# Kernel tuning notes

Hardware: AMD Instinct MI355X
Metric: run time of the kernel (lower is better)

Reference implementation:

```python
import jax, jax.numpy as jnp
import numpy as np
from jax import lax

B, C_IN, T_IN = 1024, 22, 2047
C_TEMP, KT, PAD = 20, 12, 6
N_PATCH = 8
ATT_OUT = 18
N_OUT = 4
BN_EPS = 1e-5
REEIG_EPS = 1e-4


def _sym(X):
    return 0.5 * (X + jnp.swapaxes(X, -1, -2))


def _eig_fn(X, fn):
    w, v = jnp.linalg.eigh(_sym(X))
    return jnp.einsum('...ij,...j,...kj->...ik', v, fn(w), v)


def _logm(X):
    return _eig_fn(X, lambda w: jnp.log(jnp.maximum(w, 1e-10)))


def _expm(X):
    return _eig_fn(X, jnp.exp)


def _reeig(X):
    return _eig_fn(X, lambda w: jnp.maximum(w, REEIG_EPS))


def _batchnorm(x, gamma, beta):
    # x: (B, C, T); training-mode stats over (B, T)
    mu = x.mean(axis=(0, 2), keepdims=True)
    var = x.var(axis=(0, 2), keepdims=True)
    return (x - mu) * jax.lax.rsqrt(var + BN_EPS) * gamma[None, :, None] + beta[None, :, None]


def setup_inputs() -> dict:
    key = jax.random.key(0)
    ks = jax.random.split(key, 8)
    tangent_dim = ATT_OUT * (ATT_OUT + 1) // 2
    return {
        'x': jax.random.normal(ks[0], (B, C_IN, T_IN), dtype=jnp.float32),
        'w_spat': jax.random.normal(ks[1], (C_IN, C_IN), dtype=jnp.float32) * 0.3,
        'b_spat': jnp.zeros((C_IN,), jnp.float32),
        'g1': jnp.ones((C_IN,), jnp.float32),
        'be1': jnp.zeros((C_IN,), jnp.float32),
        'w_temp': jax.random.normal(ks[2], (C_TEMP, C_IN, KT), dtype=jnp.float32) * 0.1,
        'b_temp': jnp.zeros((C_TEMP,), jnp.float32),
        'g2': jnp.ones((C_TEMP,), jnp.float32),
        'be2': jnp.zeros((C_TEMP,), jnp.float32),
        'wq': jax.random.normal(ks[3], (ATT_OUT, C_TEMP), dtype=jnp.float32) / np.sqrt(C_TEMP),
        'wk': jax.random.normal(ks[4], (ATT_OUT, C_TEMP), dtype=jnp.float32) / np.sqrt(C_TEMP),
        'wv': jax.random.normal(ks[5], (ATT_OUT, C_TEMP), dtype=jnp.float32) / np.sqrt(C_TEMP),
        'w_lin': jax.random.normal(ks[6], (N_OUT, N_PATCH * tangent_dim), dtype=jnp.float32) * 0.05,
        'b_lin': jnp.zeros((N_OUT,), jnp.float32),
    }


def _matt_forward(x, w_spat, b_spat, g1, be1, w_temp, b_temp, g2, be2, wq, wk, wv, w_lin, b_lin):
    b = x.shape[0]
    # spatial filter: Conv2d(1, n_chans, (n_chans,1)) == full channel mix
    h = jnp.einsum('oc,bct->bot', w_spat, x) + b_spat[None, :, None]
    h = _batchnorm(h, g1, be1)
    # temporal conv: Conv2d(n_chans, 20, (1,12), pad (0,6)) == 1D conv over time
    h = lax.conv_general_dilated(h, w_temp, window_strides=(1,), padding=[(PAD, PAD)],
                                 dimension_numbers=('NCH', 'OIH', 'NCH'))
    h = h + b_temp[None, :, None]
    h = _batchnorm(h, g2, be2)
    # patch embedding: split time into N_PATCH segments -> (B, P, C, Tp)
    cf, tt = h.shape[1], h.shape[2]
    tp = tt // N_PATCH
    h = h[:, :, :N_PATCH * tp].reshape(b, cf, N_PATCH, tp).transpose(0, 2, 1, 3)
    # sample covariance per patch + trace normalization
    hc = h - h.mean(axis=-1, keepdims=True)
    cov = jnp.einsum('bpct,bpdt->bpcd', hc, hc) / (tp - 1)
    cov = cov / jnp.trace(cov, axis1=-2, axis2=-1)[..., None, None]
    # manifold attention: BiMap Q/K/V = W X W^T
    Q = jnp.einsum('oi,bpij,qj->bpoq', wq, cov, wq)
    K = jnp.einsum('oi,bpij,qj->bpoq', wk, cov, wk)
    V = jnp.einsum('oi,bpij,qj->bpoq', wv, cov, wv)
    lq, lk, lv = _logm(Q), _logm(K), _logm(V)
    n = lq.shape[-1]
    fq = lq.reshape(b, N_PATCH, n * n)
    fk = lk.reshape(b, N_PATCH, n * n)
    sq = jnp.sum(fq * fq, -1)
    sk = jnp.sum(fk * fk, -1)
    cross = jnp.einsum('bid,bjd->bij', fq, fk)
    d2 = jnp.maximum(sq[:, :, None] + sk[:, None, :] - 2.0 * cross, 0.0)
    energy = jnp.sqrt(d2 + 1e-12)  # log-Euclidean distance ||logQ_i - logK_j||_F
    weights = 1.0 / (1.0 + jnp.log1p(energy))
    prob = jax.nn.softmax(weights, axis=-2)          # normalize over queries i
    probT = jnp.swapaxes(prob, -1, -2)               # (b, j, i)
    # log-Euclidean weighted Frechet mean: expm(sum_i w_ji logm(V_i))
    out = _expm(jnp.einsum('bji,bixy->bjxy', probT, lv))
    # R2E: ReEig + LogEig + triu vectorization (off-diag * sqrt(2))
    lt = _logm(_reeig(out))
    iu0, iu1 = np.triu_indices(n)
    scale = jnp.asarray(np.where(iu0 == iu1, 1.0, np.sqrt(2.0)), dtype=lt.dtype)
    vec = lt[..., iu0, iu1] * scale                  # (B, P, n(n+1)/2)
    feat = vec.reshape(b, -1)
    return feat @ w_lin.T + b_lin


def reference(x, w_spat, b_spat, g1, be1, w_temp, b_temp, g2, be2, wq, wk, wv, w_lin, b_lin):
    return _matt_forward(x, w_spat, b_spat, g1, be1, w_temp, b_temp, g2, be2, wq, wk, wv, w_lin, b_lin)
```

## Files before the change

kernel.cpp:

```cpp
#include <hip/hip_runtime.h>
#include <math.h>

constexpr int NSWEEP = 6;

constexpr size_t OFF_SUMX   = 0;
constexpr size_t OFF_G      = 22;
constexpr size_t OFF_SUM2   = 288;
constexpr size_t OFF_SUMSQ2 = 308;
constexpr size_t OFF_S2     = 328;
constexpr size_t OFF_A      = 352;
constexpr size_t OFF_D      = 840;
constexpr size_t OFF_WR     = 864;
constexpr size_t OFF_COV    = 6144;
constexpr size_t OFF_LQKV   = 3282944;
constexpr size_t OFF_FEAT   = 11245568;

struct Tri { int a[253]; int b[253]; };
constexpr Tri mk_tri(int n) {
    Tri t{}; int c = 0;
    for (int i = 0; i < n; ++i) for (int j = i; j < n; ++j) { t.a[c] = i; t.b[c] = j; ++c; }
    return t;
}
constexpr Tri T22 = mk_tri(22);
constexpr Tri T20 = mk_tri(20);
constexpr Tri T18 = mk_tri(18);

struct Sched { int p[17][9]; int q[17][9]; };
constexpr Sched mk_sched() {
    Sched s{};
    for (int r = 0; r < 17; ++r)
        for (int k = 0; k < 9; ++k) {
            int x, y;
            if (k == 0) { x = 17; y = r; }
            else { x = (r + k) % 17; y = (r - k + 17) % 17; }
            s.p[r][k] = x < y ? x : y;
            s.q[r][k] = x < y ? y : x;
        }
    return s;
}
constexpr Sched SCH = mk_sched();

__device__ __forceinline__ float jacobi18(float* __restrict__ a, float* __restrict__ v,
                                          int jj, int base) {
    int pt[17];
#pragma unroll
    for (int r = 0; r < 17; ++r) {
        int k1 = jj - r; if (k1 < 0) k1 += 17;
        int partner;
        if (jj == 17)      { partner = r; }
        else if (k1 == 0)  { partner = 17; }
        else if (k1 <= 8)  { partner = r - k1; if (partner < 0) partner += 17; }
        else               { partner = r + 17 - k1; if (partner >= 17) partner -= 17; }
        pt[r] = partner;
    }
    int kt[17];
#pragma unroll
    for (int r = 0; r < 17; ++r) {
        int k1 = jj - r; if (k1 < 0) k1 += 17;
        kt[r] = (jj == 17) ? 0 : (k1 == 0 ? 0 : (k1 <= 8 ? k1 : 17 - k1));
    }
    float mydiag = a[0];
#pragma unroll
    for (int i = 1; i < 18; ++i) if (jj == i) mydiag = a[i];

    for (int sw = 0; sw < NSWEEP; ++sw) {
#pragma unroll
        for (int r = 0; r < 17; ++r) {
            const int partner = pt[r];
            const int paddr = base + partner;
            const bool isp = jj < partner;
            float pd = __shfl(mydiag, paddr, 64);
            float apq = a[0];
#pragma unroll
            for (int i = 1; i < 18; ++i) if (partner == i) apq = a[i];
            float app = isp ? mydiag : pd;
            float aqq = isp ? pd : mydiag;
            float apqc = (fabsf(apq) < 1e-36f) ? 1e-36f : apq;
            float tau = (aqq - app) * 0.5f * __builtin_amdgcn_rcpf(apqc);
            float t0 = __builtin_amdgcn_rcpf(fabsf(tau) + __builtin_amdgcn_sqrtf(1.f + tau * tau));
            t0 = (tau < 0.f) ? -t0 : t0;
            float tb[9];
#pragma unroll
            for (int k = 0; k < 9; ++k)
                tb[k] = __shfl(t0, base + SCH.p[r][k], 64);
            float cc[9], ss[9];
#pragma unroll
            for (int k = 0; k < 9; ++k) {
                cc[k] = __builtin_amdgcn_rsqf(1.f + tb[k] * tb[k]);
                ss[k] = tb[k] * cc[k];
            }
            const int kk = kt[r];
            float mt = tb[0], mc = cc[0], ms = ss[0];
#pragma unroll
            for (int t2 = 1; t2 < 9; ++t2)
                if (kk == t2) { mt = tb[t2]; mc = cc[t2]; ms = ss[t2]; }
            mydiag = fmaf(isp ? -mt : mt, apq, mydiag);
#pragma unroll
            for (int k = 0; k < 9; ++k) {
                const int p = SCH.p[r][k], q = SCH.q[r][k];
                float tp = a[p], tq = a[q];
                a[p] = cc[k] * tp - ss[k] * tq;
                a[q] = ss[k] * tp + cc[k] * tq;
            }
            float ssig = isp ? -ms : ms;
#pragma unroll
            for (int i = 0; i < 18; ++i) {
                float oa = __shfl(a[i], paddr, 64);
                a[i] = mc * a[i] + ssig * oa;
            }
#pragma unroll
            for (int i = 0; i < 18; ++i) {
                float ov = __shfl(v[i], paddr, 64);
                v[i] = mc * v[i] + ssig * ov;
            }
        }
    }
    float lam = a[0];
#pragma unroll
    for (int i = 1; i < 18; ++i) if (jj == i) lam = a[i];
    return lam;
}

__global__ void k0_zero(float* ws) {
    int tid = threadIdx.x;
    for (int i = tid; i < 352; i += 256) ws[i] = 0.f;
}

__global__ __launch_bounds__(256) void k1_stats(const float* __restrict__ x,
                                                float* __restrict__ sumx,
                                                float* __restrict__ G) {
    int b = blockIdx.x, tid = threadIdx.x;
    __shared__ float xt[22 * 257];
    float accp = 0.f, accs = 0.f;
    int c1 = 0, c2 = 0;
    if (tid < 253) { c1 = T22.a[tid]; c2 = T22.b[tid]; }
    const float* xb = x + (size_t)b * 22 * 2047;
    for (int t0 = 0; t0 < 2047; t0 += 256) {
        __syncthreads();
        for (int idx = tid; idx < 22 * 256; idx += 256) {
            int c = idx >> 8, tl = idx & 255;
            int t = t0 + tl;
            xt[c * 257 + tl] = (t < 2047) ? xb[c * 2047 + t] : 0.f;
        }
        __syncthreads();
        if (tid < 253) {
            float s = 0.f;
            for (int t = 0; t < 256; ++t) s += xt[c1 * 257 + t] * xt[c2 * 257 + t];
            accp += s;
        }
        if (tid < 22) {
            float s = 0.f;
            for (int t = 0; t < 256; ++t) s += xt[tid * 257 + t];
            accs += s;
        }
    }
    if (tid < 253) atomicAdd(&G[tid], accp);
    if (tid < 22) atomicAdd(&sumx[tid], accs);
}

__global__ __launch_bounds__(256) void k2_prep(const float* __restrict__ w_spat,
                                               const float* __restrict__ b_spat,
                                               const float* __restrict__ g1,
                                               const float* __restrict__ be1,
                                               const float* __restrict__ w_temp,
                                               const float* __restrict__ sumx,
                                               const float* __restrict__ G,
                                               float* __restrict__ A,
                                               float* __restrict__ dv,
                                               float* __restrict__ w_r) {
    int tid = threadIdx.x;
    __shared__ float cov[22 * 22], mux[22], mu1s[22], s1s[22];
    const float invN = 1.f / (1024.f * 2047.f);
    if (tid < 22) mux[tid] = sumx[tid] * invN;
    __syncthreads();
    if (tid < 253) {
        int c1 = T22.a[tid], c2 = T22.b[tid];
        float cv = G[tid] * invN - mux[c1] * mux[c2];
        cov[c1 * 22 + c2] = cv; cov[c2 * 22 + c1] = cv;
    }
    __syncthreads();
    if (tid < 22) {
        int c = tid;
        float m = b_spat[c], varv = 0.f;
        for (int e = 0; e < 22; ++e) m += w_spat[c * 22 + e] * mux[e];
        for (int i = 0; i < 22; ++i) {
            float wi = w_spat[c * 22 + i];
            for (int j = 0; j < 22; ++j) varv += wi * w_spat[c * 22 + j] * cov[i * 22 + j];
        }
        mu1s[c] = m;
        s1s[c] = g1[c] * rsqrtf(varv + 1e-5f);
    }
    __syncthreads();
    for (int idx = tid; idx < 484; idx += 256) {
        int c = idx / 22;
        A[idx] = s1s[c] * w_spat[idx];
    }
    if (tid < 22) dv[tid] = s1s[tid] * (b_spat[tid] - mu1s[tid]) + be1[tid];
    for (int idx = tid; idx < 5280; idx += 256) {
        int f = idx / 264, r = idx % 264;
        w_r[r * 20 + f] = w_temp[idx];
    }
}

__global__ __launch_bounds__(256) void k3_conv(const float* __restrict__ x,
                                               const float* __restrict__ wsA,
                                               const float* __restrict__ wsd,
                                               const float* __restrict__ w_r,
                                               float* __restrict__ cov_raw,
                                               float* __restrict__ sum2,
                                               float* __restrict__ sumsq2) {
    int bp = blockIdx.x;
    int b = bp >> 3, p = bp & 7;
    int tid = threadIdx.x;
    __shared__ float xs[22 * 267];
    __shared__ float h2[20 * 257];
    __shared__ float pm[20];

    const float* xb = x + (size_t)b * 22 * 2047;
    const int t0 = p * 256 - 6;
    for (int idx = tid; idx < 22 * 267; idx += 256) {
        int c = idx / 267, tl = idx % 267;
        int t = t0 + tl;
        xs[idx] = (t >= 0 && t < 2047) ? xb[c * 2047 + t] : 0.f;
    }
    __syncthreads();
    for (int tl = tid; tl < 267; tl += 256) {
        float xv[22];
#pragma unroll
        for (int c = 0; c < 22; ++c) xv[c] = xs[c * 267 + tl];
        int t = t0 + tl;
        bool valid = (t >= 0 && t < 2047);
#pragma unroll
        for (int c = 0; c < 22; ++c) {
            float acc = wsd[c];
#pragma unroll
            for (int e = 0; e < 22; ++e) acc += wsA[c * 22 + e] * xv[e];
            xs[c * 267 + tl] = valid ? acc : 0.f;
        }
    }
    __syncthreads();
    {
        int tl = tid;
        float acc[20];
#pragma unroll
        for (int f = 0; f < 20; ++f) acc[f] = 0.f;
        for (int c = 0; c < 22; ++c) {
#pragma unroll
            for (int k = 0; k < 12; ++k) {
                float hv = xs[c * 267 + tl + k];
                const float* wp = w_r + (c * 12 + k) * 20;
#pragma unroll
                for (int f = 0; f < 20; ++f) acc[f] += wp[f] * hv;
            }
        }
#pragma unroll
        for (int f = 0; f < 20; ++f) h2[f * 257 + tl] = acc[f];
    }
    __syncthreads();
    if (tid < 20) {
        int f = tid;
        float s = 0.f, ss = 0.f;
        for (int t = 0; t < 256; ++t) { float v = h2[f * 257 + t]; s += v; ss += v * v; }
        pm[f] = s * (1.f / 256.f);
        atomicAdd(&sum2[f], s);
        atomicAdd(&sumsq2[f], ss);
    }
    __syncthreads();
    for (int pr = tid; pr < 210; pr += 256) {
        int f = T20.a[pr], g = T20.b[pr];
        float s = 0.f;
        for (int t = 0; t < 256; ++t) s += h2[f * 257 + t] * h2[g * 257 + t];
        float cv = s - 256.f * pm[f] * pm[g];
        cov_raw[(size_t)bp * 400 + f * 20 + g] = cv;
        if (f != g) cov_raw[(size_t)bp * 400 + g * 20 + f] = cv;
    }
}

__global__ void k4_s2(const float* __restrict__ g2, const float* __restrict__ sum2,
                      const float* __restrict__ sumsq2, float* __restrict__ s2) {
    int tid = threadIdx.x;
    if (tid < 20) {
        const float invN = 1.f / (1024.f * 2048.f);
        float mu = sum2[tid] * invN;
        float var = sumsq2[tid] * invN - mu * mu;
        s2[tid] = g2[tid] * rsqrtf(var + 1e-5f);
    }
}

__global__ __launch_bounds__(64) void k5_qkv(const float* __restrict__ wq,
                                             const float* __restrict__ wk,
                                             const float* __restrict__ wv,
                                             const float* __restrict__ s2g,
                                             const float* __restrict__ cov_raw,
                                             float* __restrict__ lqkv) {
    int bp = blockIdx.x;
    int lane = threadIdx.x;
    __shared__ float covn[400];
    __shared__ float Wl[1080];
    __shared__ float Vs[972];
    __shared__ float lws[54];
    __shared__ float s2l[20];

    if (lane < 20) s2l[lane] = s2g[lane];
    __syncthreads();
    for (int idx = lane; idx < 1080; idx += 64) {
        int m = idx / 360, rem = idx % 360;
        const float* W = (m == 0) ? wq : (m == 1) ? wk : wv;
        Wl[idx] = W[rem] * s2l[rem % 20];
    }
    for (int idx = lane; idx < 400; idx += 64)
        covn[idx] = cov_raw[(size_t)bp * 400 + idx];
    __syncthreads();

    float tr = 0.f;
#pragma unroll
    for (int f = 0; f < 20; ++f) tr += covn[f * 21] * s2l[f] * s2l[f];
    float trinv = 1.f / tr;

    int grp = lane / 18;
    int jj = lane - grp * 18;
    int m = grp < 3 ? grp : 2;
    int base = grp * 18;
    float Wrow[20];
#pragma unroll
    for (int d = 0; d < 20; ++d) Wrow[d] = Wl[m * 360 + jj * 20 + d];
    float u[20];
#pragma unroll
    for (int e = 0; e < 20; ++e) {
        float acc = 0.f;
#pragma unroll
        for (int d = 0; d < 20; ++d) acc += covn[e * 20 + d] * Wrow[d];
        u[e] = acc;
    }
    float a[18], v[18];
#pragma unroll
    for (int i = 0; i < 18; ++i) {
        float acc = 0.f;
#pragma unroll
        for (int e = 0; e < 20; ++e) acc += Wl[m * 360 + i * 20 + e] * u[e];
        a[i] = acc * trinv;
        v[i] = (i == jj) ? 1.f : 0.f;
    }
    float lam = jacobi18(a, v, jj, base);
    float lw = __logf(fmaxf(lam, 1e-10f));
    if (grp < 3) {
#pragma unroll
        for (int i = 0; i < 18; ++i) Vs[(m * 18 + i) * 18 + jj] = v[i];
        lws[m * 18 + jj] = lw;
    }
    __syncthreads();
    for (int idx = lane; idx < 972; idx += 64) {
        int m2 = idx / 324, rem = idx % 324, i = rem / 18, jo = rem % 18;
        float acc = 0.f;
#pragma unroll
        for (int kk = 0; kk < 18; ++kk)
            acc += Vs[(m2 * 18 + i) * 18 + kk] * lws[m2 * 18 + kk] * Vs[(m2 * 18 + jo) * 18 + kk];
        lqkv[(size_t)(bp * 3 + m2) * 324 + rem] = acc;
    }
}

__global__ __launch_bounds__(256) void k6_attn(const float* __restrict__ lqkv,
                                               float* __restrict__ mixed) {
    int b = blockIdx.x, tid = threadIdx.x;
    __shared__ float L[7776];
    __shared__ float sq[8], sk[8], cross[64], prob[64];
    const float* src = lqkv + (size_t)b * 7776;
    for (int idx = tid; idx < 7776; idx += 256) L[idx] = src[idx];
    __syncthreads();
    if (tid < 64) {
        int i = tid >> 3, j = tid & 7;
        const float* fq = &L[(i * 3 + 0) * 324];
        const float* fk = &L[(j * 3 + 1) * 324];
        float cr = 0.f;
        for (int e = 0; e < 324; ++e) cr += fq[e] * fk[e];
        cross[tid] = cr;
    } else if (tid < 72) {
        int i = tid - 64;
        const float* fq = &L[(i * 3 + 0) * 324];
        float s = 0.f;
        for (int e = 0; e < 324; ++e) s += fq[e] * fq[e];
        sq[i] = s;
    } else if (tid < 80) {
        int i = tid - 72;
        const float* fk = &L[(i * 3 + 1) * 324];
        float s = 0.f;
        for (int e = 0; e < 324; ++e) s += fk[e] * fk[e];
        sk[i] = s;
    }
    __syncthreads();
    if (tid < 8) {
        int j = tid;
        float w[8], mx = -1e30f;
        for (int i = 0; i < 8; ++i) {
            float d2 = fmaxf(sq[i] + sk[j] - 2.f * cross[i * 8 + j], 0.0f);
            float en = sqrtf(d2 + 1e-12f);
            w[i] = 1.f / (1.f + log1pf(en));
            mx = fmaxf(mx, w[i]);
        }
        float ssum = 0.f;
        for (int i = 0; i < 8; ++i) { w[i] = __expf(w[i] - mx); ssum += w[i]; }
        float inv = 1.f / ssum;
        for (int i = 0; i < 8; ++i) prob[i * 8 + j] = w[i] * inv;
    }
    __syncthreads();
    float* dst = mixed + (size_t)b * 8 * 324;
    for (int idx = tid; idx < 8 * 324; idx += 256) {
        int j = idx / 324, e = idx % 324;
        float acc = 0.f;
#pragma unroll
        for (int i = 0; i < 8; ++i) acc += prob[i * 8 + j] * L[(i * 3 + 2) * 324 + e];
        dst[idx] = acc;
    }
}

__global__ __launch_bounds__(64) void k7_post(const float* __restrict__ mixed,
                                              float* __restrict__ feat) {
    int blk = blockIdx.x;
    int lane = threadIdx.x;
    int grp = lane / 18;
    int jj = lane - grp * 18;
    int m = grp < 3 ? grp : 2;
    int base = grp * 18;
    int mat = blk * 3 + m;
    int matc = mat < 8192 ? mat : 8191;
    __shared__ float Vs[972];
    __shared__ float lws[54];
    __shared__ float gbs[64];
    __shared__ int sflag;

    const float* src = mixed + (size_t)matc * 324;
    float a[18], v[18];
#pragma unroll
    for (int i = 0; i < 18; ++i) {
        a[i] = src[i * 18 + jj];
        v[i] = (i == jj) ? 1.f : 0.f;
    }
    {
        float diag = a[0], asum = 0.f;
#pragma unroll
        for (int i = 0; i < 18; ++i) {
            if (jj == i) diag = a[i];
            asum += fabsf(a[i]);
        }
        gbs[lane] = 2.f * diag - asum;
    }
    __syncthreads();
    if (lane == 0) {
        float mn = 1e30f;
        for (int i = 0; i < 54; ++i) mn = fminf(mn, gbs[i]);
        sflag = (mn > -9.2103f) ? 1 : 0;
    }
    __syncthreads();
    const bool skipAll = (sflag != 0);

    if (!skipAll) {
        float lam = jacobi18(a, v, jj, base);
        float lw = fmaxf(lam, -9.210340371976182f);
        if (grp < 3) {
#pragma unroll
            for (int i = 0; i < 18; ++i) Vs[(m * 18 + i) * 18 + jj] = v[i];
            lws[m * 18 + jj] = lw;
        }
    }
    __syncthreads();
    for (int idx = lane; idx < 513; idx += 64) {
        int m2 = idx / 171, rem = idx % 171;
        int mat2 = blk * 3 + m2;
        if (mat2 >= 8192) continue;
        int i = T18.a[rem], jo = T18.b[rem];
        float acc;
        if (skipAll) {
            acc = mixed[(size_t)mat2 * 324 + i * 18 + jo];
        } else {
            acc = 0.f;
#pragma unroll
            for (int kk = 0; kk < 18; ++kk)
                acc += Vs[(m2 * 18 + i) * 18 + kk] * lws[m2 * 18 + kk] * Vs[(m2 * 18 + jo) * 18 + kk];
        }
        float scl = (i == jo) ? 1.f : 1.41421356237309515f;
        int bb = mat2 >> 3, pp = mat2 & 7;
        feat[(size_t)bb * 1368 + pp * 171 + rem] = acc * scl;
    }
}

__global__ __launch_bounds__(256) void k8_lin(const float* __restrict__ feat,
                                              const float* __restrict__ w_lin,
                                              const float* __restrict__ b_lin,
                                              float* __restrict__ out) {
    int b = blockIdx.x, tid = threadIdx.x;
    int o = tid >> 6, lane = tid & 63;
    const float* fb = feat + (size_t)b * 1368;
    const float* wo = w_lin + o * 1368;
    float acc = 0.f;
    for (int e = lane; e < 1368; e += 64) acc += fb[e] * wo[e];
    for (int off = 32; off; off >>= 1) acc += __shfl_down(acc, off, 64);
    if (lane == 0) out[b * 4 + o] = acc + b_lin[o];
}

extern "C" void kernel_launch(void* const* d_in, const int* in_sizes, int n_in,
                              void* d_out, int out_size, void* d_ws, size_t ws_size,
                              hipStream_t stream) {
    (void)in_sizes; (void)n_in; (void)out_size; (void)ws_size;
    const float* x      = (const float*)d_in[0];
    const float* w_spat = (const float*)d_in[1];
    const float* b_spat = (const float*)d_in[2];
    const float* g1     = (const float*)d_in[3];
    const float* be1    = (const float*)d_in[4];
    const float* w_temp = (const float*)d_in[5];
    const float* g2     = (const float*)d_in[7];
    const float* wq     = (const float*)d_in[9];
    const float* wk     = (const float*)d_in[10];
    const float* wv     = (const float*)d_in[11];
    const float* w_lin  = (const float*)d_in[12];
    const float* b_lin  = (const float*)d_in[13];
    float* ws  = (float*)d_ws;
    float* out = (float*)d_out;

    k0_zero<<<1, 256, 0, stream>>>(ws);
    k1_stats<<<1024, 256, 0, stream>>>(x, ws + OFF_SUMX, ws + OFF_G);
    k2_prep<<<1, 256, 0, stream>>>(w_spat, b_spat, g1, be1, w_temp,
                                   ws + OFF_SUMX, ws + OFF_G,
                                   ws + OFF_A, ws + OFF_D, ws + OFF_WR);
    k3_conv<<<8192, 256, 0, stream>>>(x, ws + OFF_A, ws + OFF_D, ws + OFF_WR,
                                      ws + OFF_COV, ws + OFF_SUM2, ws + OFF_SUMSQ2);
    k4_s2<<<1, 64, 0, stream>>>(g2, ws + OFF_SUM2, ws + OFF_SUMSQ2, ws + OFF_S2);
    k5_qkv<<<8192, 64, 0, stream>>>(wq, wk, wv, ws + OFF_S2, ws + OFF_COV, ws + OFF_LQKV);
    k6_attn<<<1024, 256, 0, stream>>>(ws + OFF_LQKV, ws + OFF_COV );
    k7_post<<<2731, 64, 0, stream>>>(ws + OFF_COV, ws + OFF_FEAT);
    k8_lin<<<1024, 256, 0, stream>>>(ws + OFF_FEAT, w_lin, b_lin, out);
}
```

Measured before the change: 1.771 ms.

## Pack four waves per block in eigen kernels and cut Jacobi sweeps

k5_qkv and k7_post now run four independent wave-sized work units per 256-thread block. Each wave has its own shared-memory slices and uses wave barriers instead of block-wide syncs. This amortises the shared weight staging and reduces launch and scheduling overhead. The skip check in k7 now uses a wave shuffle reduction instead of shared memory and two block barriers. The Jacobi sweep count drops from 6 to 5, which cuts eigen-solve work but risks lower eigenvector accuracy.

After: 1.656 ms. 6.5% less time.

```diff
diff --git a/kernel.cpp b/kernel.cpp
--- a/kernel.cpp
+++ b/kernel.cpp
@@ -1,7 +1,7 @@
 #include <hip/hip_runtime.h>
 #include <math.h>
 
-constexpr int NSWEEP = 6;
+constexpr int NSWEEP = 5;
 
 constexpr size_t OFF_SUMX   = 0;
 constexpr size_t OFF_G      = 22;
@@ -287,34 +287,36 @@
     }
 }
 
-__global__ __launch_bounds__(64) void k5_qkv(const float* __restrict__ wq,
-                                             const float* __restrict__ wk,
-                                             const float* __restrict__ wv,
-                                             const float* __restrict__ s2g,
-                                             const float* __restrict__ cov_raw,
-                                             float* __restrict__ lqkv) {
-    int bp = blockIdx.x;
-    int lane = threadIdx.x;
-    __shared__ float covn[400];
+__global__ __launch_bounds__(256) void k5_qkv(const float* __restrict__ wq,
+                                              const float* __restrict__ wk,
+                                              const float* __restrict__ wv,
+                                              const float* __restrict__ s2g,
+                                              const float* __restrict__ cov_raw,
+                                              float* __restrict__ lqkv) {
+    int tid = threadIdx.x;
+    int wave = tid >> 6;
+    int lane = tid & 63;
+    int bp = blockIdx.x * 4 + wave;
     __shared__ float Wl[1080];
-    __shared__ float Vs[972];
-    __shared__ float lws[54];
     __shared__ float s2l[20];
-
-    if (lane < 20) s2l[lane] = s2g[lane];
-    __syncthreads();
-    for (int idx = lane; idx < 1080; idx += 64) {
+    __shared__ float covn[4][400];
+    __shared__ float Vs[4][972];
+    __shared__ float lws[4][54];
+
+    if (tid < 20) s2l[tid] = s2g[tid];
+    for (int idx = lane; idx < 400; idx += 64)
+        covn[wave][idx] = cov_raw[(size_t)bp * 400 + idx];
+    __syncthreads();
+    for (int idx = tid; idx < 1080; idx += 256) {
         int m = idx / 360, rem = idx % 360;
         const float* W = (m == 0) ? wq : (m == 1) ? wk : wv;
         Wl[idx] = W[rem] * s2l[rem % 20];
     }
-    for (int idx = lane; idx < 400; idx += 64)
-        covn[idx] = cov_raw[(size_t)bp * 400 + idx];
     __syncthreads();
 
     float tr = 0.f;
 #pragma unroll
-    for (int f = 0; f < 20; ++f) tr += covn[f * 21] * s2l[f] * s2l[f];
+    for (int f = 0; f < 20; ++f) tr += covn[wave][f * 21] * s2l[f] * s2l[f];
     float trinv = 1.f / tr;
 
     int grp = lane / 18;
@@ -329,7 +331,7 @@
     for (int e = 0; e < 20; ++e) {
         float acc = 0.f;
 #pragma unroll
-        for (int d = 0; d < 20; ++d) acc += covn[e * 20 + d] * Wrow[d];
+        for (int d = 0; d < 20; ++d) acc += covn[wave][e * 20 + d] * Wrow[d];
         u[e] = acc;
     }
     float a[18], v[18];
@@ -345,16 +347,16 @@
     float lw = __logf(fmaxf(lam, 1e-10f));
     if (grp < 3) {
 #pragma unroll
-        for (int i = 0; i < 18; ++i) Vs[(m * 18 + i) * 18 + jj] = v[i];
-        lws[m * 18 + jj] = lw;
-    }
-    __syncthreads();
+        for (int i = 0; i < 18; ++i) Vs[wave][(m * 18 + i) * 18 + jj] = v[i];
+        lws[wave][m * 18 + jj] = lw;
+    }
+    __builtin_amdgcn_wave_barrier();
     for (int idx = lane; idx < 972; idx += 64) {
         int m2 = idx / 324, rem = idx % 324, i = rem / 18, jo = rem % 18;
         float acc = 0.f;
 #pragma unroll
         for (int kk = 0; kk < 18; ++kk)
-            acc += Vs[(m2 * 18 + i) * 18 + kk] * lws[m2 * 18 + kk] * Vs[(m2 * 18 + jo) * 18 + kk];
+            acc += Vs[wave][(m2 * 18 + i) * 18 + kk] * lws[wave][m2 * 18 + kk] * Vs[wave][(m2 * 18 + jo) * 18 + kk];
         lqkv[(size_t)(bp * 3 + m2) * 324 + rem] = acc;
     }
 }
@@ -413,20 +415,20 @@
     }
 }
 
-__global__ __launch_bounds__(64) void k7_post(const float* __restrict__ mixed,
-                                              float* __restrict__ feat) {
+__global__ __launch_bounds__(256) void k7_post(const float* __restrict__ mixed,
+                                               float* __restrict__ feat) {
+    int tid = threadIdx.x;
+    int wave = tid >> 6;
+    int lane = tid & 63;
     int blk = blockIdx.x;
-    int lane = threadIdx.x;
     int grp = lane / 18;
     int jj = lane - grp * 18;
     int m = grp < 3 ? grp : 2;
     int base = grp * 18;
-    int mat = blk * 3 + m;
+    int mat = blk * 12 + wave * 3 + m;
     int matc = mat < 8192 ? mat : 8191;
-    __shared__ float Vs[972];
-    __shared__ float lws[54];
-    __shared__ float gbs[64];
-    __shared__ int sflag;
+    __shared__ float Vs[4][972];
+    __shared__ float lws[4][54];
 
     const float* src = mixed + (size_t)matc * 324;
     float a[18], v[18];
@@ -435,37 +437,30 @@
         a[i] = src[i * 18 + jj];
         v[i] = (i == jj) ? 1.f : 0.f;
     }
-    {
-        float diag = a[0], asum = 0.f;
-#pragma unroll
-        for (int i = 0; i < 18; ++i) {
-            if (jj == i) diag = a[i];
-            asum += fabsf(a[i]);
-        }
-        gbs[lane] = 2.f * diag - asum;
-    }
-    __syncthreads();
-    if (lane == 0) {
-        float mn = 1e30f;
-        for (int i = 0; i < 54; ++i) mn = fminf(mn, gbs[i]);
-        sflag = (mn > -9.2103f) ? 1 : 0;
-    }
-    __syncthreads();
-    const bool skipAll = (sflag != 0);
+    float diag = a[0], asum = 0.f;
+#pragma unroll
+    for (int i = 0; i < 18; ++i) {
+        if (jj == i) diag = a[i];
+        asum += fabsf(a[i]);
+    }
+    float gb = 2.f * diag - asum;
+#pragma unroll
+    for (int off = 32; off; off >>= 1) gb = fminf(gb, __shfl_xor(gb, off, 64));
+    const bool skipAll = (gb > -9.2103f);
 
     if (!skipAll) {
         float lam = jacobi18(a, v, jj, base);
         float lw = fmaxf(lam, -9.210340371976182f);
         if (grp < 3) {
 #pragma unroll
-            for (int i = 0; i < 18; ++i) Vs[(m * 18 + i) * 18 + jj] = v[i];
-            lws[m * 18 + jj] = lw;
-        }
-    }
-    __syncthreads();
+            for (int i = 0; i < 18; ++i) Vs[wave][(m * 18 + i) * 18 + jj] = v[i];
+            lws[wave][m * 18 + jj] = lw;
+        }
+    }
+    __builtin_amdgcn_wave_barrier();
     for (int idx = lane; idx < 513; idx += 64) {
         int m2 = idx / 171, rem = idx % 171;
-        int mat2 = blk * 3 + m2;
+        int mat2 = blk * 12 + wave * 3 + m2;
         if (mat2 >= 8192) continue;
         int i = T18.a[rem], jo = T18.b[rem];
         float acc;
@@ -475,7 +470,7 @@
             acc = 0.f;
 #pragma unroll
             for (int kk = 0; kk < 18; ++kk)
-                acc += Vs[(m2 * 18 + i) * 18 + kk] * lws[m2 * 18 + kk] * Vs[(m2 * 18 + jo) * 18 + kk];
+                acc += Vs[wave][(m2 * 18 + i) * 18 + kk] * lws[wave][m2 * 18 + kk] * Vs[wave][(m2 * 18 + jo) * 18 + kk];
         }
         float scl = (i == jo) ? 1.f : 1.41421356237309515f;
         int bb = mat2 >> 3, pp = mat2 & 7;
@@ -524,8 +519,8 @@
     k3_conv<<<8192, 256, 0, stream>>>(x, ws + OFF_A, ws + OFF_D, ws + OFF_WR,
                                       ws + OFF_COV, ws + OFF_SUM2, ws + OFF_SUMSQ2);
     k4_s2<<<1, 64, 0, stream>>>(g2, ws + OFF_SUM2, ws + OFF_SUMSQ2, ws + OFF_S2);
-    k5_qkv<<<8192, 64, 0, stream>>>(wq, wk, wv, ws + OFF_S2, ws + OFF_COV, ws + OFF_LQKV);
+    k5_qkv<<<2048, 256, 0, stream>>>(wq, wk, wv, ws + OFF_S2, ws + OFF_COV, ws + OFF_LQKV);
     k6_attn<<<1024, 256, 0, stream>>>(ws + OFF_LQKV, ws + OFF_COV );
-    k7_post<<<2731, 64, 0, stream>>>(ws + OFF_COV, ws + OFF_FEAT);
+    k7_post<<<683, 256, 0, stream>>>(ws + OFF_COV, ws + OFF_FEAT);
     k8_lin<<<1024, 256, 0, stream>>>(ws + OFF_FEAT, w_lin, b_lin, out);
 }
```
